# Kernel tuning notes

Hardware: AMD Instinct MI355X
Metric: run time of the kernel (lower is better)

The kernel has to match this reference:

```python
import jax, jax.numpy as jnp
import numpy as np

N_NODES = 50000
N_EDGES = 600000
EMB = 128


def setup_inputs() -> dict:
    key = jax.random.key(0)
    ks = jax.random.split(key, 12)
    x = jax.random.normal(ks[0], (N_NODES, 8), dtype=jnp.float32)
    src = jax.random.randint(ks[1], (N_EDGES,), 0, N_NODES)
    dst = jax.random.randint(ks[2], (N_EDGES,), 0, N_NODES)
    def glorot(k, shape):
        fan = shape[0] + shape[1]
        return jax.random.normal(k, shape, dtype=jnp.float32) * jnp.sqrt(2.0 / fan)
    return {
        "x": x, "src": src, "dst": dst,
        "W1l": glorot(ks[3], (8, EMB)), "W1r": glorot(ks[4], (8, EMB)), "b1": jnp.zeros((EMB,), jnp.float32),
        "W2l": glorot(ks[5], (EMB, EMB)), "W2r": glorot(ks[6], (EMB, EMB)), "b2": jnp.zeros((EMB,), jnp.float32),
        "W3l": glorot(ks[7], (EMB, EMB)), "W3r": glorot(ks[8], (EMB, EMB)), "b3": jnp.zeros((EMB,), jnp.float32),
    }


def _sage_conv(x, src, dst, Wl, bl, Wr, deg_inv):
    # mean aggregation over incoming edges (SpMM), then lin_l(agg) + lin_r(x)
    agg = jax.ops.segment_sum(x[src], dst, num_segments=N_NODES)  # [N, d_in]
    agg = agg * deg_inv[:, None]
    return agg @ Wl + bl + x @ Wr


def reference(x, src, dst, W1l, W1r, b1, W2l, W2r, b2, W3l, W3r, b3):
    deg = jax.ops.segment_sum(jnp.ones((N_EDGES,), x.dtype), dst, num_segments=N_NODES)
    deg_inv = jnp.where(deg > 0, 1.0 / jnp.maximum(deg, 1.0), 0.0)
    h = jax.nn.relu(_sage_conv(x, src, dst, W1l, b1, W1r, deg_inv))
    h = jax.nn.relu(_sage_conv(h, src, dst, W2l, b2, W2r, deg_inv) + h)
    h = _sage_conv(h, src, dst, W3l, b3, W3r, deg_inv) + h
    return h
```

## Files before the change

### kernel.cpp

```cpp
#include <hip/hip_runtime.h>
#include <hip/hip_bf16.h>


#define EMB 128
#define SCAN_CHUNK 1024

typedef __attribute__((ext_vector_type(8))) short short8v;
typedef __attribute__((ext_vector_type(4))) float f32x4;

static __device__ __forceinline__ float bfbits2f(unsigned short u) {
    unsigned int x = ((unsigned int)u) << 16;
    return __builtin_bit_cast(float, x);
}
static __device__ __forceinline__ unsigned short f2bfbits(float f) {
    __hip_bfloat16 h = __float2bfloat16(f);
    return __builtin_bit_cast(unsigned short, h);
}


__global__ __launch_bounds__(256) void count_pack_kernel(const int* __restrict__ dst,
                                                         int* __restrict__ deg, int e, int cb,
                                                         const float* __restrict__ W2l,
                                                         const float* __restrict__ W2r,
                                                         const float* __restrict__ W3l,
                                                         const float* __restrict__ W3r,
                                                         unsigned short* __restrict__ Wp2,
                                                         unsigned short* __restrict__ Wp3) {
    if ((int)blockIdx.x < cb) {
        int i = blockIdx.x * 256 + threadIdx.x;
        if (i < e) atomicAdd(&deg[dst[i]], 1);
        return;
    }
    int t = (blockIdx.x - cb) * 256 + threadIdx.x;
    const bool second = t >= 4096;
    const float* Wl = second ? W3l : W2l;
    const float* Wr = second ? W3r : W2r;
    unsigned short* Wp = second ? Wp3 : Wp2;
    t &= 4095;
    const int s = t >> 9;
    const int ct = (t >> 6) & 7;
    const int l = t & 63;
    const int k0 = s * 32 + (l >> 4) * 8;
    const int c = ct * 16 + (l & 15);
    unsigned short frag[8];
#pragma unroll
    for (int i = 0; i < 8; ++i) {
        const int k = k0 + i;
        const float v = (k < 128) ? Wl[(size_t)k * EMB + c] : Wr[(size_t)(k - 128) * EMB + c];
        frag[i] = f2bfbits(v);
    }
    *(short8v*)(Wp + (size_t)t * 8) = *(const short8v*)frag;
}

__device__ __forceinline__ int wave_incl_scan(int v, int lane) {
#pragma unroll
    for (int off = 1; off < 64; off <<= 1) {
        int u = __shfl_up(v, off);
        if (lane >= off) v += u;
    }
    return v;
}

__global__ __launch_bounds__(256) void partial_sum_kernel(const int* __restrict__ deg,
                                                          int* __restrict__ partials, int n) {
    const int t = threadIdx.x;
    const int base = blockIdx.x * SCAN_CHUNK + t * 4;
    int s = 0;
    if (base + 3 < n) {
        int4 v = *(const int4*)(deg + base);
        s = v.x + v.y + v.z + v.w;
    } else {
        for (int i = 0; i < 4; ++i)
            if (base + i < n) s += deg[base + i];
    }
    const int lane = t & 63, wid = t >> 6;
#pragma unroll
    for (int off = 32; off > 0; off >>= 1) s += __shfl_down(s, off);
    __shared__ int wsum[4];
    if (lane == 0) wsum[wid] = s;
    __syncthreads();
    if (t == 0) partials[blockIdx.x] = wsum[0] + wsum[1] + wsum[2] + wsum[3];
}

__global__ __launch_bounds__(256) void scan_final_kernel(const int* __restrict__ deg,
                                                         const int* __restrict__ partials,
                                                         int* __restrict__ row_ptr,
                                                         int* __restrict__ cursor,
                                                         float* __restrict__ deg_inv,
                                                         int n, int nb) {
    const int t = threadIdx.x;
    const int base = blockIdx.x * SCAN_CHUNK + t * 4;
    int d[4] = {0, 0, 0, 0};
    if (base + 3 < n) {
        int4 v = *(const int4*)(deg + base);
        d[0] = v.x; d[1] = v.y; d[2] = v.z; d[3] = v.w;
    } else {
        for (int i = 0; i < 4; ++i)
            if (base + i < n) d[i] = deg[base + i];
    }
    const int tsum = d[0] + d[1] + d[2] + d[3];
    const int lane = t & 63, wid = t >> 6;
    int incl = wave_incl_scan(tsum, lane);
    __shared__ int wsum[4];
    __shared__ int s_blkoff, s_total;
    if (lane == 63) wsum[wid] = incl;
    if (t < 64) {
        int v = (t < nb) ? partials[t] : 0;
        int pincl = wave_incl_scan(v, t);
        if (t == (int)blockIdx.x) s_blkoff = pincl - v;
        if (t == nb - 1) s_total = pincl;
    }
    __syncthreads();
    int off = s_blkoff;
    for (int w = 0; w < wid; ++w) off += wsum[w];
    int run = off + incl - tsum;
#pragma unroll
    for (int i = 0; i < 4; ++i) {
        int idx = base + i;
        if (idx < n) {
            row_ptr[idx] = run;
            cursor[idx] = run;
            deg_inv[idx] = (d[i] > 0) ? 1.0f / (float)d[i] : 0.0f;
            run += d[i];
        }
    }
    if (blockIdx.x == 0 && t == 0) row_ptr[n] = s_total;
}

__global__ void fill_csr_kernel(const int* __restrict__ src, const int* __restrict__ dst,
                                int* __restrict__ cursor, int* __restrict__ edge_src, int e) {
    int i = blockIdx.x * blockDim.x + threadIdx.x;
    if (i < e) {
        int p = atomicAdd(&cursor[dst[i]], 1);
        edge_src[p] = src[i];
    }
}


__global__ __launch_bounds__(256) void fused_l1_kernel(const float* __restrict__ x,
                                                       const int* __restrict__ row_ptr,
                                                       const int* __restrict__ edge_src,
                                                       const float* __restrict__ deg_inv,
                                                       const float* __restrict__ W1l,
                                                       const float* __restrict__ W1r,
                                                       const float* __restrict__ bias,
                                                       unsigned short* __restrict__ outb,
                                                       int n) {
    __shared__ float As[32][8];
    __shared__ float Bs[32][8];
    const int t = threadIdx.x;
    const int rb = blockIdx.x * 32;

    {
        const int node8 = t >> 3;
        const int ch = t & 7;
        const int node = rb + node8;
        float a = 0.f, bsv = 0.f, di = 0.f;
        if (node < n) {
            const int s0 = row_ptr[node], s1 = row_ptr[node + 1];
            for (int e = s0; e < s1; e += 4) {
                const int sa = edge_src[e];
                const int sb = edge_src[min(e + 1, s1 - 1)];
                const int sc = edge_src[min(e + 2, s1 - 1)];
                const int sd = edge_src[min(e + 3, s1 - 1)];
                const float f1 = (e + 1 < s1) ? 1.f : 0.f;
                const float f2 = (e + 2 < s1) ? 1.f : 0.f;
                const float f3 = (e + 3 < s1) ? 1.f : 0.f;
                a += x[(size_t)sa * 8 + ch];
                a = fmaf(f1, x[(size_t)sb * 8 + ch], a);
                a = fmaf(f2, x[(size_t)sc * 8 + ch], a);
                a = fmaf(f3, x[(size_t)sd * 8 + ch], a);
            }
            di = deg_inv[node];
            bsv = x[(size_t)node * 8 + ch];
        }
        As[node8][ch] = a * di;
        Bs[node8][ch] = bsv;
    }
    __syncthreads();

    const int tx = t & 31;
    const int ty = t >> 5;
    const int c0 = tx * 4;

    const float4 bv = *(const float4*)(bias + c0);
    float4 acc[4] = {bv, bv, bv, bv};

#pragma unroll
    for (int k = 0; k < 8; k += 4) {
        float4 a4[4], b4[4];
#pragma unroll
        for (int i = 0; i < 4; ++i) {
            a4[i] = *(const float4*)&As[ty + 8 * i][k];
            b4[i] = *(const float4*)&Bs[ty + 8 * i][k];
        }
#pragma unroll
        for (int kk = 0; kk < 4; ++kk) {
            const float4 wl = *(const float4*)(W1l + (size_t)(k + kk) * EMB + c0);
            const float4 wr = *(const float4*)(W1r + (size_t)(k + kk) * EMB + c0);
#pragma unroll
            for (int i = 0; i < 4; ++i) {
                const float av = ((const float*)&a4[i])[kk];
                const float bw = ((const float*)&b4[i])[kk];
                acc[i].x = fmaf(av, wl.x, acc[i].x);
                acc[i].y = fmaf(av, wl.y, acc[i].y);
                acc[i].z = fmaf(av, wl.z, acc[i].z);
                acc[i].w = fmaf(av, wl.w, acc[i].w);
                acc[i].x = fmaf(bw, wr.x, acc[i].x);
                acc[i].y = fmaf(bw, wr.y, acc[i].y);
                acc[i].z = fmaf(bw, wr.z, acc[i].z);
                acc[i].w = fmaf(bw, wr.w, acc[i].w);
            }
        }
    }

#pragma unroll
    for (int i = 0; i < 4; ++i) {
        int r = rb + ty + 8 * i;
        if (r < n) {
            float4 v = acc[i];
            v.x = fmaxf(v.x, 0.f); v.y = fmaxf(v.y, 0.f);
            v.z = fmaxf(v.z, 0.f); v.w = fmaxf(v.w, 0.f);
            unsigned long long pk = (unsigned long long)f2bfbits(v.x) |
                                    ((unsigned long long)f2bfbits(v.y) << 16) |
                                    ((unsigned long long)f2bfbits(v.z) << 32) |
                                    ((unsigned long long)f2bfbits(v.w) << 48);
            *(unsigned long long*)(outb + (size_t)r * EMB + c0) = pk;
        }
    }
}


__global__ __launch_bounds__(256) void agg128_bf16_kernel(const unsigned short* __restrict__ hb,
                                                          const int* __restrict__ row_ptr,
                                                          const int* __restrict__ edge_src,
                                                          const float* __restrict__ deg_inv,
                                                          unsigned short* __restrict__ aggb,
                                                          int n) {
    const int wave = threadIdx.x >> 6;
    const int lane = threadIdx.x & 63;
    const int half = lane >> 5;
    const int cl = lane & 31;
    const int node = blockIdx.x * 4 + wave;
    if (node >= n) return;
    const int s0 = row_ptr[node];
    const int s1 = row_ptr[node + 1];
    const size_t coff = (size_t)cl * 4;
    float a0 = 0.f, a1 = 0.f, a2 = 0.f, a3 = 0.f;
    for (int e = s0 + half; e < s1; e += 8) {
        const int sa = edge_src[e];
        const int sb = edge_src[min(e + 2, s1 - 1)];
        const int sc = edge_src[min(e + 4, s1 - 1)];
        const int sd = edge_src[min(e + 6, s1 - 1)];
        const float f1 = (e + 2 < s1) ? 1.f : 0.f;
        const float f2 = (e + 4 < s1) ? 1.f : 0.f;
        const float f3 = (e + 6 < s1) ? 1.f : 0.f;
        const uint2 va = *(const uint2*)(hb + (size_t)sa * EMB + coff);
        const uint2 vb = *(const uint2*)(hb + (size_t)sb * EMB + coff);
        const uint2 vc = *(const uint2*)(hb + (size_t)sc * EMB + coff);
        const uint2 vd = *(const uint2*)(hb + (size_t)sd * EMB + coff);
        a0 += bfbits2f((unsigned short)va.x);
        a1 += bfbits2f((unsigned short)(va.x >> 16));
        a2 += bfbits2f((unsigned short)va.y);
        a3 += bfbits2f((unsigned short)(va.y >> 16));
        a0 = fmaf(f1, bfbits2f((unsigned short)vb.x), a0);
        a1 = fmaf(f1, bfbits2f((unsigned short)(vb.x >> 16)), a1);
        a2 = fmaf(f1, bfbits2f((unsigned short)vb.y), a2);
        a3 = fmaf(f1, bfbits2f((unsigned short)(vb.y >> 16)), a3);
        a0 = fmaf(f2, bfbits2f((unsigned short)vc.x), a0);
        a1 = fmaf(f2, bfbits2f((unsigned short)(vc.x >> 16)), a1);
        a2 = fmaf(f2, bfbits2f((unsigned short)vc.y), a2);
        a3 = fmaf(f2, bfbits2f((unsigned short)(vc.y >> 16)), a3);
        a0 = fmaf(f3, bfbits2f((unsigned short)vd.x), a0);
        a1 = fmaf(f3, bfbits2f((unsigned short)(vd.x >> 16)), a1);
        a2 = fmaf(f3, bfbits2f((unsigned short)vd.y), a2);
        a3 = fmaf(f3, bfbits2f((unsigned short)(vd.y >> 16)), a3);
    }
    a0 += __shfl_xor(a0, 32);
    a1 += __shfl_xor(a1, 32);
    a2 += __shfl_xor(a2, 32);
    a3 += __shfl_xor(a3, 32);
    if (half == 0) {
        const float di = deg_inv[node];
        uint2 o;
        o.x = (unsigned int)f2bfbits(a0 * di) | ((unsigned int)f2bfbits(a1 * di) << 16);
        o.y = (unsigned int)f2bfbits(a2 * di) | ((unsigned int)f2bfbits(a3 * di) << 16);
        *(uint2*)(aggb + (size_t)node * EMB + coff) = o;
    }
}


template <bool RELU, bool WRITEB, bool SKIPB>
__global__ __launch_bounds__(256) void mfma_gemm_kernel(const unsigned short* __restrict__ Ab,
                                                        const unsigned short* __restrict__ Hb,
                                                        const unsigned short* __restrict__ Wp,
                                                        const float* __restrict__ bias,
                                                        const float* skipf,
                                                        const unsigned short* skipb,
                                                        float* outf,
                                                        unsigned short* __restrict__ outb,
                                                        int n) {
    const int l = threadIdx.x & 63;
    const int w = threadIdx.x >> 6;
    const int rowbase = blockIdx.x * 64 + w * 16;
    const int lr = l & 15;
    const int lg = l >> 4;

    int r0 = rowbase + lr;
    if (r0 > n - 1) r0 = n - 1;
    const size_t arow = (size_t)r0 * EMB + lg * 8;

    f32x4 acc[8] = {};

#pragma unroll
    for (int s = 0; s < 8; ++s) {
        const unsigned short* abase = (s < 4) ? (Ab + arow + s * 32)
                                              : (Hb + arow + (s - 4) * 32);
        const short8v af = *(const short8v*)abase;
        const unsigned short* wbase = Wp + ((size_t)(s * 8) * 64 + l) * 8;
#pragma unroll
        for (int ct = 0; ct < 8; ++ct) {
            const short8v bfr = *(const short8v*)(wbase + (size_t)ct * 64 * 8);
            acc[ct] = __builtin_amdgcn_mfma_f32_16x16x32_bf16(af, bfr, acc[ct], 0, 0, 0);
        }
    }

#pragma unroll
    for (int ct = 0; ct < 8; ++ct) {
        const int c = ct * 16 + lr;
        const float bv = bias[c];
#pragma unroll
        for (int j = 0; j < 4; ++j) {
            const int r = rowbase + lg * 4 + j;
            if (r < n) {
                const float sk = SKIPB ? bfbits2f(skipb[(size_t)r * EMB + c])
                                       : skipf[(size_t)r * EMB + c];
                float v = acc[ct][j] + bv + sk;
                if (RELU) v = fmaxf(v, 0.f);
                outf[(size_t)r * EMB + c] = v;
                if (WRITEB) outb[(size_t)r * EMB + c] = f2bfbits(v);
            }
        }
    }
}


extern "C" void kernel_launch(void* const* d_in, const int* in_sizes, int n_in,
                              void* d_out, int out_size, void* d_ws, size_t ws_size,
                              hipStream_t stream) {
    const float* x   = (const float*)d_in[0];
    const int*   src = (const int*)d_in[1];
    const int*   dst = (const int*)d_in[2];
    const float* W1l = (const float*)d_in[3];
    const float* W1r = (const float*)d_in[4];
    const float* b1  = (const float*)d_in[5];
    const float* W2l = (const float*)d_in[6];
    const float* W2r = (const float*)d_in[7];
    const float* b2  = (const float*)d_in[8];
    const float* W3l = (const float*)d_in[9];
    const float* W3r = (const float*)d_in[10];
    const float* b3  = (const float*)d_in[11];
    float* out = (float*)d_out;

    const int N = in_sizes[0] / 8;
    const int E = in_sizes[1];

    char* ws = (char*)d_ws;
    const size_t hbytes  = (size_t)N * EMB * sizeof(float);
    const size_t hbbytes = (size_t)N * EMB * sizeof(unsigned short);
    float* h2f = (float*)ws;
    unsigned short* h1b  = (unsigned short*)(ws + hbytes);
    unsigned short* h2b  = (unsigned short*)(ws + hbytes + hbbytes);
    unsigned short* aggb = (unsigned short*)(ws + hbytes + 2 * hbbytes);
    char* p = ws + hbytes + 3 * hbbytes;
    unsigned short* Wp2 = (unsigned short*)p;  p += 4096 * 8 * sizeof(unsigned short);
    unsigned short* Wp3 = (unsigned short*)p;  p += 4096 * 8 * sizeof(unsigned short);
    int* deg      = (int*)p;
    int* row_ptr  = deg + N;
    int* cursor   = row_ptr + N + 1;
    float* deg_inv = (float*)(cursor + N);
    int* edge_src = (int*)(deg_inv + N);
    int* partials = edge_src + E;

    const int nb = (N + SCAN_CHUNK - 1) / SCAN_CHUNK;
    const int cb = (E + 255) / 256;

    hipMemsetAsync(deg, 0, (size_t)N * sizeof(int), stream);
    count_pack_kernel<<<cb + 32, 256, 0, stream>>>(dst, deg, E, cb,
                                                   W2l, W2r, W3l, W3r, Wp2, Wp3);
    partial_sum_kernel<<<nb, 256, 0, stream>>>(deg, partials, N);
    scan_final_kernel<<<nb, 256, 0, stream>>>(deg, partials, row_ptr, cursor, deg_inv, N, nb);
    fill_csr_kernel<<<cb, 256, 0, stream>>>(src, dst, cursor, edge_src, E);

    const int agg_grid  = (N + 3) / 4;
    const int mfma_grid = (N + 63) / 64;

    fused_l1_kernel<<<(N + 31) / 32, 256, 0, stream>>>(
        x, row_ptr, edge_src, deg_inv, W1l, W1r, b1, h1b, N);

    agg128_bf16_kernel<<<agg_grid, 256, 0, stream>>>(h1b, row_ptr, edge_src, deg_inv, aggb, N);
    mfma_gemm_kernel<true, true, true><<<mfma_grid, 256, 0, stream>>>(
        aggb, h1b, Wp2, b2, nullptr, h1b, h2f, h2b, N);

    agg128_bf16_kernel<<<agg_grid, 256, 0, stream>>>(h2b, row_ptr, edge_src, deg_inv, aggb, N);
    mfma_gemm_kernel<false, false, false><<<mfma_grid, 256, 0, stream>>>(
        aggb, h2b, Wp3, b3, h2f, nullptr, out, nullptr, N);
}
```

Baseline: 189.0 us.

## Fuse CSR build stages into one cooperative kernel with grid syncs

Replaces the memset, degree-count/weight-pack, two scan kernels and CSR fill kernel with a single cooperative launch whose phases are separated by grid.sync(). The edge loops now handle four edges per thread through int4 loads of dst and src. The aim is to cut per-launch overhead and inter-kernel gaps in the preprocessing. In exchange it pays for grid-wide barriers, and it falls back to the old multi-kernel path if the cooperative launch fails.

```diff
diff --git a/kernel.cpp b/kernel.cpp
--- a/kernel.cpp
+++ b/kernel.cpp
@@ -1,9 +1,12 @@
 #include <hip/hip_runtime.h>
 #include <hip/hip_bf16.h>
+#include <hip/hip_cooperative_groups.h>
 
 
 #define EMB 128
 #define SCAN_CHUNK 1024
+
+namespace cg = cooperative_groups;
 
 typedef __attribute__((ext_vector_type(8))) short short8v;
 typedef __attribute__((ext_vector_type(4))) float f32x4;
@@ -15,6 +18,154 @@
 static __device__ __forceinline__ unsigned short f2bfbits(float f) {
     __hip_bfloat16 h = __float2bfloat16(f);
     return __builtin_bit_cast(unsigned short, h);
+}
+
+__device__ __forceinline__ int wave_incl_scan(int v, int lane) {
+#pragma unroll
+    for (int off = 1; off < 64; off <<= 1) {
+        int u = __shfl_up(v, off);
+        if (lane >= off) v += u;
+    }
+    return v;
+}
+
+static __device__ __forceinline__ void pack_one(int t, const float* __restrict__ Wl,
+                                                const float* __restrict__ Wr,
+                                                unsigned short* __restrict__ Wp) {
+    const int s = t >> 9;
+    const int ct = (t >> 6) & 7;
+    const int l = t & 63;
+    const int k0 = s * 32 + (l >> 4) * 8;
+    const int c = ct * 16 + (l & 15);
+    unsigned short frag[8];
+#pragma unroll
+    for (int i = 0; i < 8; ++i) {
+        const int k = k0 + i;
+        const float v = (k < 128) ? Wl[(size_t)k * EMB + c] : Wr[(size_t)(k - 128) * EMB + c];
+        frag[i] = f2bfbits(v);
+    }
+    *(short8v*)(Wp + (size_t)t * 8) = *(const short8v*)frag;
+}
+
+
+__global__ __launch_bounds__(256) void coop_csr_kernel(const int* __restrict__ src,
+                                                       const int* __restrict__ dst,
+                                                       int* __restrict__ deg,
+                                                       int* __restrict__ row_ptr,
+                                                       int* __restrict__ cursor,
+                                                       float* __restrict__ deg_inv,
+                                                       int* __restrict__ edge_src,
+                                                       int* __restrict__ partials,
+                                                       int n, int e, int nb, int cb,
+                                                       const float* __restrict__ W2l,
+                                                       const float* __restrict__ W2r,
+                                                       const float* __restrict__ W3l,
+                                                       const float* __restrict__ W3r,
+                                                       unsigned short* __restrict__ Wp2,
+                                                       unsigned short* __restrict__ Wp3) {
+    cg::grid_group grid = cg::this_grid();
+    const int t = threadIdx.x;
+    const int tid = blockIdx.x * 256 + t;
+    __shared__ int wsum[4];
+    __shared__ int s_blkoff, s_total;
+
+    {
+        const int nq = n >> 2;
+        if (tid < nq) ((int4*)deg)[tid] = make_int4(0, 0, 0, 0);
+        if (tid == 0)
+            for (int i = nq << 2; i < n; ++i) deg[i] = 0;
+    }
+    grid.sync();
+
+    if ((int)blockIdx.x < cb) {
+        const int eq = e >> 2;
+        if (tid < eq) {
+            const int4 d4 = ((const int4*)dst)[tid];
+            atomicAdd(&deg[d4.x], 1);
+            atomicAdd(&deg[d4.y], 1);
+            atomicAdd(&deg[d4.z], 1);
+            atomicAdd(&deg[d4.w], 1);
+        }
+        if (tid == 0)
+            for (int i = eq << 2; i < e; ++i) atomicAdd(&deg[dst[i]], 1);
+    } else if ((int)blockIdx.x < cb + 32) {
+        const int pt = ((int)blockIdx.x - cb) * 256 + t;
+        if (pt < 4096) pack_one(pt, W2l, W2r, Wp2);
+        else           pack_one(pt - 4096, W3l, W3r, Wp3);
+    }
+    grid.sync();
+
+    if ((int)blockIdx.x < nb) {
+        const int base = blockIdx.x * SCAN_CHUNK + t * 4;
+        int s = 0;
+        if (base + 3 < n) {
+            int4 v = *(const int4*)(deg + base);
+            s = v.x + v.y + v.z + v.w;
+        } else {
+            for (int i = 0; i < 4; ++i)
+                if (base + i < n) s += deg[base + i];
+        }
+        const int lane = t & 63, wid = t >> 6;
+#pragma unroll
+        for (int off = 32; off > 0; off >>= 1) s += __shfl_down(s, off);
+        if (lane == 0) wsum[wid] = s;
+        __syncthreads();
+        if (t == 0) partials[blockIdx.x] = wsum[0] + wsum[1] + wsum[2] + wsum[3];
+    }
+    grid.sync();
+
+    if ((int)blockIdx.x < nb) {
+        const int base = blockIdx.x * SCAN_CHUNK + t * 4;
+        int d[4] = {0, 0, 0, 0};
+        if (base + 3 < n) {
+            int4 v = *(const int4*)(deg + base);
+            d[0] = v.x; d[1] = v.y; d[2] = v.z; d[3] = v.w;
+        } else {
+            for (int i = 0; i < 4; ++i)
+                if (base + i < n) d[i] = deg[base + i];
+        }
+        const int tsum = d[0] + d[1] + d[2] + d[3];
+        const int lane = t & 63, wid = t >> 6;
+        int incl = wave_incl_scan(tsum, lane);
+        if (lane == 63) wsum[wid] = incl;
+        if (t < 64) {
+            int v = (t < nb) ? partials[t] : 0;
+            int pincl = wave_incl_scan(v, t);
+            if (t == (int)blockIdx.x) s_blkoff = pincl - v;
+            if (t == nb - 1) s_total = pincl;
+        }
+        __syncthreads();
+        int off = s_blkoff;
+        for (int w = 0; w < wid; ++w) off += wsum[w];
+        int run = off + incl - tsum;
+#pragma unroll
+        for (int i = 0; i < 4; ++i) {
+            int idx = base + i;
+            if (idx < n) {
+                row_ptr[idx] = run;
+                cursor[idx] = run;
+                deg_inv[idx] = (d[i] > 0) ? 1.0f / (float)d[i] : 0.0f;
+                run += d[i];
+            }
+        }
+        if (blockIdx.x == 0 && t == 0) row_ptr[n] = s_total;
+    }
+    grid.sync();
+
+    {
+        const int eq = e >> 2;
+        if (tid < eq) {
+            const int4 d4 = ((const int4*)dst)[tid];
+            const int4 s4 = ((const int4*)src)[tid];
+            edge_src[atomicAdd(&cursor[d4.x], 1)] = s4.x;
+            edge_src[atomicAdd(&cursor[d4.y], 1)] = s4.y;
+            edge_src[atomicAdd(&cursor[d4.z], 1)] = s4.z;
+            edge_src[atomicAdd(&cursor[d4.w], 1)] = s4.w;
+        }
+        if (tid == 0)
+            for (int i = eq << 2; i < e; ++i)
+                edge_src[atomicAdd(&cursor[dst[i]], 1)] = src[i];
+    }
 }
 
 
@@ -31,34 +182,9 @@
         if (i < e) atomicAdd(&deg[dst[i]], 1);
         return;
     }
-    int t = (blockIdx.x - cb) * 256 + threadIdx.x;
-    const bool second = t >= 4096;
-    const float* Wl = second ? W3l : W2l;
-    const float* Wr = second ? W3r : W2r;
-    unsigned short* Wp = second ? Wp3 : Wp2;
-    t &= 4095;
-    const int s = t >> 9;
-    const int ct = (t >> 6) & 7;
-    const int l = t & 63;
-    const int k0 = s * 32 + (l >> 4) * 8;
-    const int c = ct * 16 + (l & 15);
-    unsigned short frag[8];
-#pragma unroll
-    for (int i = 0; i < 8; ++i) {
-        const int k = k0 + i;
-        const float v = (k < 128) ? Wl[(size_t)k * EMB + c] : Wr[(size_t)(k - 128) * EMB + c];
-        frag[i] = f2bfbits(v);
-    }
-    *(short8v*)(Wp + (size_t)t * 8) = *(const short8v*)frag;
-}
-
-__device__ __forceinline__ int wave_incl_scan(int v, int lane) {
-#pragma unroll
-    for (int off = 1; off < 64; off <<= 1) {
-        int u = __shfl_up(v, off);
-        if (lane >= off) v += u;
-    }
-    return v;
+    int pt = ((int)blockIdx.x - cb) * 256 + threadIdx.x;
+    if (pt < 4096) pack_one(pt, W2l, W2r, Wp2);
+    else           pack_one(pt - 4096, W3l, W3r, Wp3);
 }
 
 __global__ __launch_bounds__(256) void partial_sum_kernel(const int* __restrict__ deg,
@@ -383,14 +509,30 @@
     int* partials = edge_src + E;
 
     const int nb = (N + SCAN_CHUNK - 1) / SCAN_CHUNK;
-    const int cb = (E + 255) / 256;
-
-    hipMemsetAsync(deg, 0, (size_t)N * sizeof(int), stream);
-    count_pack_kernel<<<cb + 32, 256, 0, stream>>>(dst, deg, E, cb,
-                                                   W2l, W2r, W3l, W3r, Wp2, Wp3);
-    partial_sum_kernel<<<nb, 256, 0, stream>>>(deg, partials, N);
-    scan_final_kernel<<<nb, 256, 0, stream>>>(deg, partials, row_ptr, cursor, deg_inv, N, nb);
-    fill_csr_kernel<<<cb, 256, 0, stream>>>(src, dst, cursor, edge_src, E);
+    const int cbq = ((E >> 2) + 255) / 256;
+
+    {
+        int n_ = N, e_ = E, nb_ = nb, cb_ = cbq;
+        void* args[] = {(void*)&src, (void*)&dst, (void*)&deg, (void*)&row_ptr,
+                        (void*)&cursor, (void*)&deg_inv, (void*)&edge_src, (void*)&partials,
+                        (void*)&n_, (void*)&e_, (void*)&nb_, (void*)&cb_,
+                        (void*)&W2l, (void*)&W2r, (void*)&W3l, (void*)&W3r,
+                        (void*)&Wp2, (void*)&Wp3};
+        const int coop_grid = cbq + 32;
+        hipError_t err = hipLaunchCooperativeKernel((void*)coop_csr_kernel,
+                                                    dim3(coop_grid), dim3(256),
+                                                    args, 0, stream);
+        if (err != hipSuccess) {
+            const int cb = (E + 255) / 256;
+            hipMemsetAsync(deg, 0, (size_t)N * sizeof(int), stream);
+            count_pack_kernel<<<cb + 32, 256, 0, stream>>>(dst, deg, E, cb,
+                                                           W2l, W2r, W3l, W3r, Wp2, Wp3);
+            partial_sum_kernel<<<nb, 256, 0, stream>>>(deg, partials, N);
+            scan_final_kernel<<<nb, 256, 0, stream>>>(deg, partials, row_ptr, cursor,
+                                                      deg_inv, N, nb);
+            fill_csr_kernel<<<cb, 256, 0, stream>>>(src, dst, cursor, edge_src, E);
+        }
+    }
 
     const int agg_grid  = (N + 3) / 4;
     const int mfma_grid = (N + 63) / 64;
```

New measurement: 447.7 us. 137% more time.
